# Performance work log

Hardware: AMD Instinct MI355X
Metric: run time of the kernel (lower is better)

Reference implementation:

```python
import jax, jax.numpy as jnp
import numpy as np

N_QUBITS = 8
N_QLAYERS = 2
D_MODEL = 8
NUM_HEADS = 2
DEPTH = D_MODEL // NUM_HEADS


def _apply_1q(state, U, wire):
    # state: (T, 2, 2, ..., 2); U: (2, 2) complex
    state = jnp.moveaxis(state, 1 + wire, -1)
    state = jnp.einsum('...b,ab->...a', state, U)
    return jnp.moveaxis(state, -1, 1 + wire)


def _apply_cnot(state, ctrl, tgt):
    s = jnp.moveaxis(state, (1 + ctrl, 1 + tgt), (-2, -1))
    s = jnp.concatenate([s[..., :1, :], s[..., 1:, ::-1]], axis=-2)
    return jnp.moveaxis(s, (-2, -1), (1 + ctrl, 1 + tgt))


def _z_signs(n):
    idx = jnp.arange(2 ** n)
    bits = (idx[:, None] >> jnp.arange(n - 1, -1, -1)[None, :]) & 1  # col i = qubit i
    return (1.0 - 2.0 * bits).astype(jnp.float32)  # (2^n, n)


def quantum_circuit(x, w):
    """AngleEmbedding(RX) + BasicEntanglerLayers(RX + CNOT ring) + PauliZ expvals.
    x: (T, n) float angles; w: (L, n) float weights -> (T, n) float expvals."""
    T, n = x.shape
    L = w.shape[0]
    # AngleEmbedding: RX(x_i)|0> = cos(x_i/2)|0> - i sin(x_i/2)|1>; product state
    h = 0.5 * x
    amps = jnp.stack([jnp.cos(h).astype(jnp.complex64),
                      (-1j) * jnp.sin(h).astype(jnp.complex64)], axis=-1)  # (T, n, 2)
    state = amps[:, 0, :]
    for i in range(1, n):
        state = (state[:, :, None] * amps[:, i, None, :]).reshape(T, -1)
    state = state.reshape((T,) + (2,) * n)
    for l in range(L):
        for i in range(n):
            th = 0.5 * w[l, i]
            cc = jnp.cos(th).astype(jnp.complex64)
            ss = (-1j) * jnp.sin(th).astype(jnp.complex64)
            U = jnp.stack([jnp.stack([cc, ss]), jnp.stack([ss, cc])])  # RX(w)
            state = _apply_1q(state, U, i)
        pairs = [(i, (i + 1) % n) for i in range(n)] if n > 2 else [(0, 1)]
        for c, t in pairs:
            state = _apply_cnot(state, c, t)
    probs = jnp.abs(state.reshape(T, -1)) ** 2  # (T, 2^n)
    return probs @ _z_signs(n)  # (T, n)


def setup_inputs() -> dict:
    key = jax.random.key(0)
    ks = jax.random.split(key, 8)
    B, S, d = 32, 1024, D_MODEL
    q = jax.random.normal(ks[0], (B, S, d), dtype=jnp.float32)
    k = jax.random.normal(ks[1], (B, S, d), dtype=jnp.float32)
    v = jax.random.normal(ks[2], (B, S, d), dtype=jnp.float32)
    mask = jnp.triu(jnp.ones((S, S), dtype=jnp.float32), k=1)[None, None]  # causal
    weights_q = jax.random.uniform(ks[3], (N_QLAYERS, N_QUBITS), dtype=jnp.float32, maxval=2 * np.pi)
    weights_k = jax.random.uniform(ks[4], (N_QLAYERS, N_QUBITS), dtype=jnp.float32, maxval=2 * np.pi)
    weights_v = jax.random.uniform(ks[5], (N_QLAYERS, N_QUBITS), dtype=jnp.float32, maxval=2 * np.pi)
    weights_dense = jax.random.uniform(ks[6], (N_QLAYERS, N_QUBITS), dtype=jnp.float32, maxval=2 * np.pi)
    return {"q": q, "k": k, "v": v, "mask": mask,
            "weights_q": weights_q, "weights_k": weights_k,
            "weights_v": weights_v, "weights_dense": weights_dense}


def reference(q, k, v, mask, weights_q, weights_k, weights_v, weights_dense):
    B, S, d = q.shape
    T = B * S
    # per-token quantum Q/K/V embeddings (batched over all B*S tokens)
    qe = quantum_circuit(q.reshape(T, d), weights_q).reshape(B, S, d)
    ke = quantum_circuit(k.reshape(T, d), weights_k).reshape(B, S, d)
    ve = quantum_circuit(v.reshape(T, d), weights_v).reshape(B, S, d)
    # split heads: (B, H, S, depth)
    def split(x):
        return x.reshape(B, S, NUM_HEADS, DEPTH).transpose(0, 2, 1, 3)
    qh, kh, vh = split(qe), split(ke), split(ve)
    scores = jnp.einsum('bhqd,bhkd->bhqk', qh, kh) / jnp.sqrt(jnp.float32(DEPTH))
    scores = scores + mask * (-1e9)
    attn = jax.nn.softmax(scores, axis=-1)
    ctx = jnp.einsum('bhqk,bhkd->bhqd', attn, vh)
    ctx = ctx.transpose(0, 2, 1, 3).reshape(B, S, d)
    out = quantum_circuit(ctx.reshape(T, d), weights_dense).reshape(B, S, d)
    return out, attn
```

## Files before the change

### kernel.cpp

```cpp
#include <hip/hip_runtime.h>

#define S_LEN 1024
#define BATCH 32
#define NHEAD 2
#define HDIM  4


#define TBL_STRIDE 256

__global__ __launch_bounds__(256)
void pauli_setup(const float* __restrict__ wq, const float* __restrict__ wk,
                 const float* __restrict__ wv, const float* __restrict__ wd,
                 float4* __restrict__ tables, int* __restrict__ counts)
{
    int blk = blockIdx.x;
    int set = blk >> 3, w = blk & 7;
    const float* wt = (set == 0) ? wq : (set == 1) ? wk : (set == 2) ? wv : wd;

    float c2[8], s2[8];
#pragma unroll
    for (int j = 0; j < 8; ++j) {
        float th = wt[8 + j];
        s2[j] = __sinf(th);
        c2[j] = __cosf(th);
    }

    unsigned X = 0u, Z = 1u << w;
    int sg0 = 0;
#pragma unroll
    for (int g = 7; g >= 0; --g) {
        int c = g, t = (g + 1) & 7;
        unsigned xc = (X >> c) & 1u, zt = (Z >> t) & 1u;
        unsigned xt = (X >> t) & 1u, zc = (Z >> c) & 1u;
        sg0 ^= (int)(xc & zt & (xt ^ zc ^ 1u));
        X ^= xc << t;
        Z ^= zt << c;
    }

    int tid = threadIdx.x;
    float coef = sg0 ? -1.0f : 1.0f;
    unsigned Xb = X;
    int k = 0;
#pragma unroll
    for (int j = 0; j < 8; ++j) {
        if ((Z >> j) & 1u) {
            int bit = (tid >> k) & 1;
            ++k;
            if (!((X >> j) & 1u)) {
                if (bit) { Xb |= 1u << j; coef *= s2[j]; }
                else     { coef *= c2[j]; }
            } else {
                if (bit) { Xb &= ~(1u << j); coef *= -s2[j]; }
                else     { coef *= c2[j]; }
            }
        }
    }
    bool valid = (tid < (1 << k));

    unsigned Xf = Xb, Zf = Z;
    int sg = 0;
#pragma unroll
    for (int g = 7; g >= 0; --g) {
        int c = g, t = (g + 1) & 7;
        unsigned xc = (Xf >> c) & 1u, zt = (Zf >> t) & 1u;
        unsigned xt = (Xf >> t) & 1u, zc = (Zf >> c) & 1u;
        sg ^= (int)(xc & zt & (xt ^ zc ^ 1u));
        Xf ^= xc << t;
        Zf ^= zt << c;
    }

    bool keep = valid && ((Xf & ~Zf) == 0u);
    if (sg ^ (__popc(Xf) & 1)) coef = -coef;
    unsigned zonly = Zf & ~Xf;
    unsigned ymask = Xf;

    __shared__ int wsum[4];
    int lane = tid & 63, wvx = tid >> 6;
    unsigned long long mb = __ballot((int)keep);
    if (lane == 0) wsum[wvx] = __popcll(mb);
    __syncthreads();
    int prefix = 0;
#pragma unroll
    for (int i = 0; i < 4; ++i)
        if (i < wvx) prefix += wsum[i];
    int pos = prefix + __popcll(mb & ((1ull << lane) - 1ull));
    if (keep) {
        float4 t4;
        t4.x = __int_as_float((int)zonly);
        t4.y = __int_as_float((int)ymask);
        t4.z = coef;
        t4.w = 0.0f;
        tables[blk * TBL_STRIDE + pos] = t4;
    }
    __syncthreads();
    if (tid == 0) counts[blk] = wsum[0] + wsum[1] + wsum[2] + wsum[3];
}

__global__ __launch_bounds__(256)
void qc_eval(const float* __restrict__ x0, const float* __restrict__ w0a,
             const float* __restrict__ x1, const float* __restrict__ w0b,
             const float* __restrict__ x2, const float* __restrict__ w0c,
             const float4* __restrict__ tables, const int* __restrict__ counts,
             float* __restrict__ o0, float* __restrict__ o1, float* __restrict__ o2,
             int rows_per_seg, int set_base)
{
    int gr = blockIdx.x * 256 + threadIdx.x;
    int seg = gr / rows_per_seg;
    int row = gr - seg * rows_per_seg;
    const float* x  = (seg == 0) ? x0 : (seg == 1) ? x1 : x2;
    const float* w0 = (seg == 0) ? w0a : (seg == 1) ? w0b : w0c;
    float*       o  = (seg == 0) ? o0 : (seg == 1) ? o1 : o2;
    int set = set_base + seg;

    const float4* xp = reinterpret_cast<const float4*>(x + (size_t)row * 8);
    float4 xa = xp[0], xb = xp[1];
    float cc[8], ss[8];
    {
        float a;
        a = xa.x + w0[0]; __sincosf(a, &ss[0], &cc[0]);
        a = xa.y + w0[1]; __sincosf(a, &ss[1], &cc[1]);
        a = xa.z + w0[2]; __sincosf(a, &ss[2], &cc[2]);
        a = xa.w + w0[3]; __sincosf(a, &ss[3], &cc[3]);
        a = xb.x + w0[4]; __sincosf(a, &ss[4], &cc[4]);
        a = xb.y + w0[5]; __sincosf(a, &ss[5], &cc[5]);
        a = xb.z + w0[6]; __sincosf(a, &ss[6], &cc[6]);
        a = xb.w + w0[7]; __sincosf(a, &ss[7], &cc[7]);
    }

    float res[8];
#pragma unroll
    for (int w = 0; w < 8; ++w) {
        int blk = set * 8 + w;
        int cnt = counts[blk];
        const float4* base = tables + blk * TBL_STRIDE;
        float acc = 0.0f;
        for (int t = 0; t < cnt; ++t) {
            float4 T = base[t];
            unsigned zm = (unsigned)__float_as_int(T.x);
            unsigned ym = (unsigned)__float_as_int(T.y);
            float v = T.z;
#pragma unroll
            for (int m = 0; m < 8; ++m) {
                float f = ((ym >> m) & 1u) ? ss[m]
                        : (((zm >> m) & 1u) ? cc[m] : 1.0f);
                v *= f;
            }
            acc += v;
        }
        res[w] = acc;
    }

    float4* op = reinterpret_cast<float4*>(o + (size_t)row * 8);
    op[0] = make_float4(res[0], res[1], res[2], res[3]);
    op[1] = make_float4(res[4], res[5], res[6], res[7]);
}

__global__ __launch_bounds__(256, 2)
void attn_kernel(const float* qe, const float* __restrict__ ke,
                 const float* __restrict__ ve, float* __restrict__ attn,
                 float* ctx)
{
    int tid = threadIdx.x;
    int bid = blockIdx.x;
    int it  = bid & 15;
    int h   = (bid >> 4) & 1;
    int b   = bid >> 5;
    int lane = tid & 63;
    int wave = tid >> 6;

    float kR0[16], kR1[16], kR2[16], kR3[16];
    float vR0[16], vR1[16], vR2[16], vR3[16];
    const float4* ke4 = reinterpret_cast<const float4*>(ke);
    const float4* ve4 = reinterpret_cast<const float4*>(ve);
#pragma unroll
    for (int t = 0; t < 16; ++t) {
        int j = t * 64 + lane;
        float4 kk = ke4[((size_t)b * S_LEN + j) * 2 + h];
        float4 vv = ve4[((size_t)b * S_LEN + j) * 2 + h];
        kR0[t] = kk.x; kR1[t] = kk.y; kR2[t] = kk.z; kR3[t] = kk.w;
        vR0[t] = vv.x; vR1[t] = vv.y; vR2[t] = vv.z; vR3[t] = vv.w;
    }

    int i0 = it * 64 + wave * 16;

#pragma unroll 1
    for (int rr = 0; rr < 16; ++rr) {
        int i = i0 + rr;
        const float* qrow = qe + ((size_t)b * S_LEN + i) * 8 + h * HDIM;
        float q0 = qrow[0] * 0.5f, q1 = qrow[1] * 0.5f;
        float q2 = qrow[2] * 0.5f, q3 = qrow[3] * 0.5f;

        float pe[16];
        float sum = 0.0f, pv0 = 0, pv1 = 0, pv2 = 0, pv3 = 0;
#pragma unroll
        for (int t = 0; t < 16; ++t) {
            int j = t * 64 + lane;
            float s = q0 * kR0[t] + q1 * kR1[t] + q2 * kR2[t] + q3 * kR3[t];
            float p = (j <= i) ? __expf(s) : 0.0f;
            pe[t] = p;
            sum += p;
            pv0 += p * vR0[t];
            pv1 += p * vR1[t];
            pv2 += p * vR2[t];
            pv3 += p * vR3[t];
        }
#pragma unroll
        for (int m = 1; m < 64; m <<= 1) sum += __shfl_xor(sum, m);
        float inv = 1.0f / sum;

        size_t base = (((size_t)(b * NHEAD + h)) * S_LEN + i) * S_LEN;
#pragma unroll
        for (int t = 0; t < 16; ++t)
            __builtin_nontemporal_store(pe[t] * inv, &attn[base + t * 64 + lane]);

#pragma unroll
        for (int m = 1; m < 64; m <<= 1) {
            pv0 += __shfl_xor(pv0, m);
            pv1 += __shfl_xor(pv1, m);
            pv2 += __shfl_xor(pv2, m);
            pv3 += __shfl_xor(pv3, m);
        }
        if (lane == 0) {
            float* c = ctx + ((size_t)b * S_LEN + i) * 8 + h * HDIM;
            c[0] = pv0 * inv; c[1] = pv1 * inv; c[2] = pv2 * inv; c[3] = pv3 * inv;
        }
    }
}

extern "C" void kernel_launch(void* const* d_in, const int* in_sizes, int n_in,
                              void* d_out, int out_size, void* d_ws, size_t ws_size,
                              hipStream_t stream)
{
    const float* q  = (const float*)d_in[0];
    const float* k  = (const float*)d_in[1];
    const float* v  = (const float*)d_in[2];
    const float* wq = (const float*)d_in[4];
    const float* wk = (const float*)d_in[5];
    const float* wv = (const float*)d_in[6];
    const float* wd = (const float*)d_in[7];

    float* out  = (float*)d_out;
    float* attn = out + (size_t)BATCH * S_LEN * 8;

    float*  ws     = (float*)d_ws;
    float*  qe     = ws;
    float*  ke     = ws + 262144;
    float*  ve     = ws + 524288;
    float4* tables = (float4*)(ws + 786432);
    int*    counts = (int*)(ws + 786432 + 32768);

    const int rows = BATCH * S_LEN;

    pauli_setup<<<dim3(32), 256, 0, stream>>>(wq, wk, wv, wd, tables, counts);

    qc_eval<<<dim3(rows * 3 / 256), 256, 0, stream>>>(
        q, wq, k, wk, v, wv, tables, counts, qe, ke, ve, rows, 0);

    attn_kernel<<<dim3(BATCH * NHEAD * 16), 256, 0, stream>>>(qe, ke, ve, attn, qe);

    qc_eval<<<dim3(rows / 256), 256, 0, stream>>>(
        qe, wd, qe, wd, qe, wd, tables, counts, out, out, out, rows, 3);
}
```

Measured before the change: 102.7 us.

## Stage V in shared memory and raise attention kernel occupancy

The attention kernel now keeps only K in registers and loads the V rows for its batch/head into a 16 KB shared-memory buffer. The launch bound goes from 2 to 4 blocks per CU to raise occupancy. The next query row is also prefetched one iteration ahead. The aim is to cut register pressure and hide latency in a kernel bound by its attention-matrix writes, at the cost of an extra LDS read per inner-loop element and a block-wide barrier.

```diff
diff --git a/kernel.cpp b/kernel.cpp
--- a/kernel.cpp
+++ b/kernel.cpp
@@ -155,11 +155,13 @@
     op[1] = make_float4(res[4], res[5], res[6], res[7]);
 }
 
-__global__ __launch_bounds__(256, 2)
+__global__ __launch_bounds__(256, 4)
 void attn_kernel(const float* qe, const float* __restrict__ ke,
                  const float* __restrict__ ve, float* __restrict__ attn,
                  float* ctx)
 {
+    __shared__ float4 vT[S_LEN];
+
     int tid = threadIdx.x;
     int bid = blockIdx.x;
     int it  = bid & 15;
@@ -168,41 +170,47 @@
     int lane = tid & 63;
     int wave = tid >> 6;
 
-    float kR0[16], kR1[16], kR2[16], kR3[16];
-    float vR0[16], vR1[16], vR2[16], vR3[16];
-    const float4* ke4 = reinterpret_cast<const float4*>(ke);
-    const float4* ve4 = reinterpret_cast<const float4*>(ve);
-#pragma unroll
-    for (int t = 0; t < 16; ++t) {
-        int j = t * 64 + lane;
-        float4 kk = ke4[((size_t)b * S_LEN + j) * 2 + h];
-        float4 vv = ve4[((size_t)b * S_LEN + j) * 2 + h];
-        kR0[t] = kk.x; kR1[t] = kk.y; kR2[t] = kk.z; kR3[t] = kk.w;
-        vR0[t] = vv.x; vR1[t] = vv.y; vR2[t] = vv.z; vR3[t] = vv.w;
-    }
+    const float4* ke4 = reinterpret_cast<const float4*>(ke) + h;
+    const float4* ve4 = reinterpret_cast<const float4*>(ve) + h;
+    size_t rowbase = (size_t)b * S_LEN;
+
+    for (int j = tid; j < S_LEN; j += 256)
+        vT[j] = ve4[(rowbase + j) * 2];
+
+    float4 kR[16];
+#pragma unroll
+    for (int t = 0; t < 16; ++t)
+        kR[t] = ke4[(rowbase + t * 64 + lane) * 2];
+
+    __syncthreads();
 
     int i0 = it * 64 + wave * 16;
-
-#pragma unroll 1
+    const float* qp = qe + (rowbase + i0) * 8 + h * HDIM;
+
+    float4 qv = *reinterpret_cast<const float4*>(qp);
+
     for (int rr = 0; rr < 16; ++rr) {
         int i = i0 + rr;
-        const float* qrow = qe + ((size_t)b * S_LEN + i) * 8 + h * HDIM;
-        float q0 = qrow[0] * 0.5f, q1 = qrow[1] * 0.5f;
-        float q2 = qrow[2] * 0.5f, q3 = qrow[3] * 0.5f;
+        float q0 = qv.x * 0.5f, q1 = qv.y * 0.5f;
+        float q2 = qv.z * 0.5f, q3 = qv.w * 0.5f;
+        if (rr < 15)
+            qv = *reinterpret_cast<const float4*>(qp + (size_t)(rr + 1) * 8);
 
         float pe[16];
         float sum = 0.0f, pv0 = 0, pv1 = 0, pv2 = 0, pv3 = 0;
 #pragma unroll
         for (int t = 0; t < 16; ++t) {
             int j = t * 64 + lane;
-            float s = q0 * kR0[t] + q1 * kR1[t] + q2 * kR2[t] + q3 * kR3[t];
+            float4 kk = kR[t];
+            float s = q0 * kk.x + q1 * kk.y + q2 * kk.z + q3 * kk.w;
             float p = (j <= i) ? __expf(s) : 0.0f;
             pe[t] = p;
             sum += p;
-            pv0 += p * vR0[t];
-            pv1 += p * vR1[t];
-            pv2 += p * vR2[t];
-            pv3 += p * vR3[t];
+            float4 vv = vT[j];
+            pv0 += p * vv.x;
+            pv1 += p * vv.y;
+            pv2 += p * vv.z;
+            pv3 += p * vv.w;
         }
 #pragma unroll
         for (int m = 1; m < 64; m <<= 1) sum += __shfl_xor(sum, m);
@@ -221,7 +229,7 @@
             pv3 += __shfl_xor(pv3, m);
         }
         if (lane == 0) {
-            float* c = ctx + ((size_t)b * S_LEN + i) * 8 + h * HDIM;
+            float* c = ctx + (rowbase + i) * 8 + h * HDIM;
             c[0] = pv0 * inv; c[1] = pv1 * inv; c[2] = pv2 * inv; c[3] = pv3 * inv;
         }
     }
```

Result: slower. 207.8 us (+102.3%).
